# Optimization experiments

Measured on AMD Instinct MI355X. Metric: run time of the kernel, lower is better.

The kernel has to match this reference:

```python
import jax, jax.numpy as jnp
import numpy as np

N, E, G = 50000, 800000, 64
NODE_DIM, HID, HEADS, EDGE_DIM = 128, 256, 4, 2
LAYER_IN = [NODE_DIM, HID, HID]
LAYER_HEADS = [HEADS, HEADS, 1]
BN_EPS = 1e-5


def setup_inputs() -> dict:
    key = jax.random.key(0)
    ks = iter(jax.random.split(key, 80))
    def nrm(shape, s=0.05):
        return jax.random.normal(next(ks), shape, jnp.float32) * s
    inp = {}
    inp['x'] = jax.random.normal(next(ks), (N, NODE_DIM), jnp.float32)
    inp['edge_index'] = jax.random.randint(next(ks), (2, E), 0, N, jnp.int32)
    inp['edge_attr'] = jax.random.normal(next(ks), (E, EDGE_DIM), jnp.float32)
    inp['batch'] = jnp.sort(jax.random.randint(next(ks), (N,), 0, G, jnp.int32))
    for i in range(3):
        H = LAYER_HEADS[i]; C = HID // H
        inp[f'W{i}'] = nrm((LAYER_IN[i], H * C))
        inp[f'asrc{i}'] = nrm((H, C))
        inp[f'adst{i}'] = nrm((H, C))
        inp[f'We{i}'] = nrm((EDGE_DIM, H * C))
        inp[f'aedge{i}'] = nrm((H, C))
        inp[f'bconv{i}'] = jnp.zeros((HID,), jnp.float32)
        inp[f'bn{i}_g'] = jnp.ones((HID,), jnp.float32)
        inp[f'bn{i}_b'] = jnp.zeros((HID,), jnp.float32)
        inp[f'bn{i}_m'] = nrm((HID,), 0.01)
        inp[f'bn{i}_v'] = jnp.ones((HID,), jnp.float32)
    inp['Wskip'] = nrm((NODE_DIM, HID))
    inp['bskip'] = jnp.zeros((HID,), jnp.float32)
    inp['Wp1'] = nrm((2 * HID, HID))
    inp['bp1'] = jnp.zeros((HID,), jnp.float32)
    inp['Wp2'] = nrm((HID, 1))
    inp['bp2'] = jnp.zeros((1,), jnp.float32)
    return inp


def gat_conv(x, src, dst, ea, W, a_s, a_d, We, a_e, b, H, concat):
    n = x.shape[0]
    C = W.shape[1] // H
    h = (x @ W).reshape(n, H, C)                      # [N,H,C]
    # attention logits per edge (src/dst node terms + edge term)
    al = ((h * a_s).sum(-1)[src]
          + (h * a_d).sum(-1)[dst]
          + ((ea @ We).reshape(-1, H, C) * a_e).sum(-1))  # [Et,H]
    al = jax.nn.leaky_relu(al, 0.2)
    # segment softmax over destination nodes
    amax = jax.ops.segment_max(al, dst, num_segments=n)
    ex = jnp.exp(al - amax[dst])
    den = jax.ops.segment_sum(ex, dst, num_segments=n)
    alpha = ex / (den[dst] + 1e-16)
    out = jax.ops.segment_sum(h[src] * alpha[..., None], dst, num_segments=n)  # [N,H,C]
    out = out.reshape(n, H * C) if concat else out.mean(axis=1)
    return out + b


def _forward(x, edge_index, edge_attr, batch, layer_params, Wskip, bskip, Wp1, bp1, Wp2, bp2):
    n = x.shape[0]
    # add self-loops (PyG GATConv default), edge_attr filled with mean
    loop = jnp.arange(n, dtype=edge_index.dtype)
    src = jnp.concatenate([edge_index[0], loop])
    dst = jnp.concatenate([edge_index[1], loop])
    ea = jnp.concatenate([edge_attr, jnp.broadcast_to(edge_attr.mean(0), (n, edge_attr.shape[1]))], axis=0)
    identity = x
    for i, (W, a_s, a_d, We, a_e, b, g, be, rm, rv) in enumerate(layer_params):
        layer_identity = (identity @ Wskip + bskip) if i == 0 else identity
        concat = i < 2
        H = LAYER_HEADS[i]
        h = gat_conv(x, src, dst, ea, W, a_s, a_d, We, a_e, b, H, concat)
        h = (h - rm) * jax.lax.rsqrt(rv + BN_EPS) * g + be   # BatchNorm1d (eval)
        h = jax.nn.elu(h)
        x = h + layer_identity
        identity = x
    # global mean + max pool per graph
    counts = jnp.maximum(jax.ops.segment_sum(jnp.ones((n,), x.dtype), batch, num_segments=G), 1.0)
    mean_pool = jax.ops.segment_sum(x, batch, num_segments=G) / counts[:, None]
    max_pool = jax.ops.segment_max(x, batch, num_segments=G)
    emb = jnp.concatenate([mean_pool, max_pool], axis=1)      # [G, 2*HID]
    hmid = jax.nn.relu(emb @ Wp1 + bp1)
    return hmid @ Wp2 + bp2                                   # [G, 1]


def reference(x, edge_index, edge_attr, batch,
              W0, asrc0, adst0, We0, aedge0, bconv0, bn0_g, bn0_b, bn0_m, bn0_v,
              W1, asrc1, adst1, We1, aedge1, bconv1, bn1_g, bn1_b, bn1_m, bn1_v,
              W2, asrc2, adst2, We2, aedge2, bconv2, bn2_g, bn2_b, bn2_m, bn2_v,
              Wskip, bskip, Wp1, bp1, Wp2, bp2):
    layer_params = [
        (W0, asrc0, adst0, We0, aedge0, bconv0, bn0_g, bn0_b, bn0_m, bn0_v),
        (W1, asrc1, adst1, We1, aedge1, bconv1, bn1_g, bn1_b, bn1_m, bn1_v),
        (W2, asrc2, adst2, We2, aedge2, bconv2, bn2_g, bn2_b, bn2_m, bn2_v),
    ]
    return _forward(x, edge_index, edge_attr, batch, layer_params, Wskip, bskip, Wp1, bp1, Wp2, bp2)
```

## Files before the change

### kernel.cpp

```cpp
#include <hip/hip_runtime.h>
#include <cfloat>

#define Nn 50000
#define Ee 800000
#define Etot (Ee + Nn)
#define Gg 64
#define HIDc 256
#define BN_EPS 1e-5f

typedef unsigned int   uint32;
typedef unsigned short ushort16;
typedef short  bf16x8 __attribute__((ext_vector_type(8)));
typedef float  f32x4  __attribute__((ext_vector_type(4)));

__device__ inline ushort16 f2bf(float f) {
    uint32 u = __float_as_uint(f);
    u = (u + 0x7fffu + ((u >> 16) & 1u)) >> 16;
    return (ushort16)u;
}
__device__ inline uint32 pack2(float a, float b) {
    return (uint32)f2bf(a) | ((uint32)f2bf(b) << 16);
}
__device__ inline uint32 fenc(float f) {
    uint32 b = __float_as_uint(f);
    return (b & 0x80000000u) ? ~b : (b | 0x80000000u);
}
__device__ inline float fdec(uint32 u) {
    uint32 b = (u & 0x80000000u) ? (u & 0x7fffffffu) : ~u;
    return __uint_as_float(b);
}

__device__ inline long ws_index(int c, int k, int KB) {
    int cb = c >> 4, m = c & 15, kb = k >> 5, q = (k >> 3) & 3, e = k & 7;
    return (((long)(cb * KB + kb) * 64 + q * 16 + m) << 3) + e;
}

#define CVT4 (Nn * 128 / 4)
#define CVT_BLKS ((CVT4 + 255) / 256)
#define EBKS ((Etot + 255) / 256)
__global__ __launch_bounds__(256) void prep_kernel(
        const float* __restrict__ ea, float* __restrict__ ea_s,
        const float* __restrict__ We0, const float* __restrict__ ae0,
        const float* __restrict__ We1, const float* __restrict__ ae1,
        const float* __restrict__ We2, const float* __restrict__ ae2,
        float* __restrict__ M,
        const float* __restrict__ W0, const float* __restrict__ Wskip,
        const float* __restrict__ W1, const float* __restrict__ W2,
        ushort16* __restrict__ WtC, ushort16* __restrict__ Wt1,
        ushort16* __restrict__ Wt2,
        const float* __restrict__ x, ushort16* __restrict__ xbf,
        const int* __restrict__ ei, int* __restrict__ counts,
        const float* __restrict__ bc0, const float* __restrict__ g0,
        const float* __restrict__ b0, const float* __restrict__ m0,
        const float* __restrict__ v0,
        const float* __restrict__ bc1, const float* __restrict__ g1,
        const float* __restrict__ b1, const float* __restrict__ m1,
        const float* __restrict__ v1,
        const float* __restrict__ bc2, const float* __restrict__ g2,
        const float* __restrict__ b2, const float* __restrict__ m2,
        const float* __restrict__ v2,
        float* __restrict__ bnf) {
    int bid = blockIdx.x, t = threadIdx.x;
    if (bid < 256) {
        __shared__ float sh0[256], sh1[256];
        float s0 = 0.f, s1 = 0.f;
        for (int e = bid * 256 + t; e < Ee; e += 256 * 256) {
            s0 += ea[2 * e];
            s1 += ea[2 * e + 1];
        }
        sh0[t] = s0; sh1[t] = s1;
        __syncthreads();
        for (int off = 128; off > 0; off >>= 1) {
            if (t < off) { sh0[t] += sh0[t + off]; sh1[t] += sh1[t + off]; }
            __syncthreads();
        }
        if (t == 0) { atomicAdd(&ea_s[0], sh0[0]); atomicAdd(&ea_s[1], sh1[0]); }
    } else if (bid == 256) {
        if (t >= 18) return;
        int l = t < 8 ? 0 : (t < 16 ? 1 : 2);
        int r = t - l * 8;
        const float* We = (l == 0) ? We0 : (l == 1 ? We1 : We2);
        const float* ae = (l == 0) ? ae0 : (l == 1 ? ae1 : ae2);
        int Hl = (l < 2) ? 4 : 1;
        int Cl = 256 / Hl;
        int d = r / Hl, hh = r % Hl;
        float s = 0.f;
        for (int c = 0; c < Cl; ++c)
            s += We[d * 256 + hh * Cl + c] * ae[hh * Cl + c];
        M[l * 8 + r] = s;
    } else if (bid < 385) {
        int k = bid - 257;
        WtC[ws_index(t, k, 4)] = f2bf(W0[(long)k * 256 + t]);
    } else if (bid < 513) {
        int k = bid - 385;
        WtC[ws_index(256 + t, k, 4)] = f2bf(Wskip[(long)k * 256 + t]);
    } else if (bid < 769) {
        int k = bid - 513;
        Wt1[ws_index(t, k, 8)] = f2bf(W1[(long)k * 256 + t]);
    } else if (bid < 1025) {
        int k = bid - 769;
        Wt2[ws_index(t, k, 8)] = f2bf(W2[(long)k * 256 + t]);
    } else if (bid == 1025) {
        for (int ll = 0; ll < 3; ++ll) {
            const float* bc = ll == 0 ? bc0 : (ll == 1 ? bc1 : bc2);
            const float* gg = ll == 0 ? g0  : (ll == 1 ? g1  : g2);
            const float* bb = ll == 0 ? b0  : (ll == 1 ? b1  : b2);
            const float* mm = ll == 0 ? m0  : (ll == 1 ? m1  : m2);
            const float* vv = ll == 0 ? v0  : (ll == 1 ? v1  : v2);
            float s = gg[t] * rsqrtf(vv[t] + BN_EPS);
            bnf[ll * 512 + t]       = s;
            bnf[ll * 512 + 256 + t] = (bc[t] - mm[t]) * s + bb[t];
        }
    } else if (bid < 1026 + CVT_BLKS) {
        int i = (bid - 1026) * 256 + t;
        if (i < CVT4) {
            float4 v = *(const float4*)&x[i * 4];
            ushort4 o;
            o.x = f2bf(v.x); o.y = f2bf(v.y); o.z = f2bf(v.z); o.w = f2bf(v.w);
            *(ushort4*)&xbf[i * 4] = o;
        }
    } else {
        int e = (bid - 1026 - CVT_BLKS) * 256 + t;
        if (e < Etot) {
            int d = (e < Ee) ? ei[Ee + e] : (e - Ee);
            atomicAdd(&counts[d], 1);
        }
    }
}

__global__ void scan1_kernel(const int* __restrict__ in, int* __restrict__ inc,
                             int* __restrict__ bsums) {
    __shared__ int sh[256];
    int i = blockIdx.x * 256 + threadIdx.x;
    int v = (i < Nn) ? in[i] : 0;
    sh[threadIdx.x] = v;
    __syncthreads();
    for (int off = 1; off < 256; off <<= 1) {
        int t = ((int)threadIdx.x >= off) ? sh[threadIdx.x - off] : 0;
        __syncthreads();
        sh[threadIdx.x] += t;
        __syncthreads();
    }
    if (i < Nn) inc[i] = sh[threadIdx.x];
    if (threadIdx.x == 255) bsums[blockIdx.x] = sh[255];
}

__global__ void scan23_kernel(const int* __restrict__ inc, const int* __restrict__ bsums,
                              int* __restrict__ row_start, int* __restrict__ cursor, int nb) {
    __shared__ int sh[256];
    int b = blockIdx.x, t = threadIdx.x;
    sh[t] = (t < b && t < nb) ? bsums[t] : 0;
    __syncthreads();
    for (int off = 128; off > 0; off >>= 1) {
        if (t < off) sh[t] += sh[t + off];
        __syncthreads();
    }
    int base = sh[0];
    int i = b * 256 + t;
    if (i < Nn) {
        int v = inc[i] + base;
        row_start[i + 1] = v;
        cursor[i + 1] = v;
    }
    if (i == 0) { row_start[0] = 0; cursor[0] = 0; }
}

__global__ void scatter_kernel(const int* __restrict__ ei, const float* __restrict__ ea,
                               const float* __restrict__ ea_sum, int* __restrict__ cursor,
                               int* __restrict__ src_sorted, float* __restrict__ ea_sorted) {
    int e = blockIdx.x * blockDim.x + threadIdx.x;
    if (e >= Etot) return;
    int s, d; float e0, e1;
    if (e < Ee) {
        s = ei[e]; d = ei[Ee + e];
        e0 = ea[2 * e]; e1 = ea[2 * e + 1];
    } else {
        s = d = e - Ee;
        const float invE = 1.f / (float)Ee;
        e0 = ea_sum[0] * invE; e1 = ea_sum[1] * invE;
    }
    int pos = atomicAdd(&cursor[d], 1);
    src_sorted[pos] = s;
    ea_sorted[2 * pos]     = e0;
    ea_sorted[2 * pos + 1] = e1;
}

#define LDK0 136
__global__ __launch_bounds__(512) void mfma_gemm0_kernel(
        const ushort16* __restrict__ A,
        const ushort16* __restrict__ WS,
        uint32* __restrict__ outF, uint32* __restrict__ outS,
        const float* __restrict__ bskip,
        const float* __restrict__ a_s, const float* __restrict__ a_d,
        float* __restrict__ ssrc, float* __restrict__ sdst, int n) {
    __shared__ ushort16 As[128 * LDK0];
    const int t = threadIdx.x;
    const int row0 = blockIdx.x * 128;
    const int wave = t >> 6, lane = t & 63;
    const int wr = wave >> 2, wc = wave & 3;
    const int l15 = lane & 15, quad = lane >> 4;

    {
        int sm = t & 127, q4 = t >> 7;
        int grow = row0 + sm;
#pragma unroll
        for (int h = 0; h < 4; ++h) {
            int oct = q4 * 4 + h;
            uint4 va = make_uint4(0, 0, 0, 0);
            if (grow < n) va = *(const uint4*)&A[(long)grow * 128 + 8 * oct];
            *(uint4*)&As[sm * LDK0 + 8 * oct] = va;
        }
    }
    __syncthreads();

    for (int cc = 0; cc < 2; ++cc) {
        const int c0 = cc * 256;
        const bool isSkip = (cc == 1);
        f32x4 acc[4][4];
#pragma unroll
        for (int j = 0; j < 4; ++j)
#pragma unroll
            for (int i = 0; i < 4; ++i) {
                acc[j][i][0] = 0.f; acc[j][i][1] = 0.f;
                acc[j][i][2] = 0.f; acc[j][i][3] = 0.f;
            }
#pragma unroll
        for (int kb = 0; kb < 4; ++kb) {
            bf16x8 bfv[4];
#pragma unroll
            for (int j = 0; j < 4; ++j) {
                int cb = ((c0 + wc * 64) >> 4) + j;
                bfv[j] = *(const bf16x8*)&WS[(((long)cb * 4 + kb) * 64 + lane) << 3];
            }
            bf16x8 af[4];
#pragma unroll
            for (int i = 0; i < 4; ++i)
                af[i] = *(const bf16x8*)&As[(wr * 64 + i * 16 + l15) * LDK0
                                            + kb * 32 + quad * 8];
#pragma unroll
            for (int j = 0; j < 4; ++j)
#pragma unroll
                for (int i = 0; i < 4; ++i)
                    acc[j][i] = __builtin_amdgcn_mfma_f32_16x16x32_bf16(
                        bfv[j], af[i], acc[j][i], 0, 0, 0);
        }

        float4 bb[4];
#pragma unroll
        for (int j = 0; j < 4; ++j) {
            if (isSkip) bb[j] = *(const float4*)&bskip[wc * 64 + j * 16 + quad * 4];
            else        bb[j] = make_float4(0.f, 0.f, 0.f, 0.f);
        }
        uint32* tgt = isSkip ? outS : outF;
#pragma unroll
        for (int i = 0; i < 4; ++i) {
            int row = row0 + wr * 64 + i * 16 + l15;
            if (row >= n) continue;
#pragma unroll
            for (int j = 0; j < 4; ++j) {
                int col = wc * 64 + j * 16 + quad * 4;
                uint2 pk;
                pk.x = pack2(acc[j][i][0] + bb[j].x, acc[j][i][1] + bb[j].y);
                pk.y = pack2(acc[j][i][2] + bb[j].z, acc[j][i][3] + bb[j].w);
                *(uint2*)&tgt[(long)row * 128 + (col >> 1)] = pk;
            }
        }

        if (!isSkip) {
            float4 asv[4], adv[4];
#pragma unroll
            for (int j = 0; j < 4; ++j) {
                int col = wc * 64 + j * 16 + quad * 4;
                asv[j] = *(const float4*)&a_s[col];
                adv[j] = *(const float4*)&a_d[col];
            }
#pragma unroll
            for (int i = 0; i < 4; ++i) {
                float ps = 0.f, pd = 0.f;
#pragma unroll
                for (int j = 0; j < 4; ++j) {
                    ps += acc[j][i][0] * asv[j].x + acc[j][i][1] * asv[j].y
                        + acc[j][i][2] * asv[j].z + acc[j][i][3] * asv[j].w;
                    pd += acc[j][i][0] * adv[j].x + acc[j][i][1] * adv[j].y
                        + acc[j][i][2] * adv[j].z + acc[j][i][3] * adv[j].w;
                }
                ps += __shfl_xor(ps, 16); ps += __shfl_xor(ps, 32);
                pd += __shfl_xor(pd, 16); pd += __shfl_xor(pd, 32);
                if (quad == 0) {
                    int row = row0 + wr * 64 + i * 16 + l15;
                    if (row < n) {
                        ssrc[row * 4 + wc] = ps;
                        sdst[row * 4 + wc] = pd;
                    }
                }
            }
        }
    }
}

#define LDK 40
__global__ __launch_bounds__(512) void mfma_gemm12_kernel(
        const ushort16* __restrict__ A,
        const ushort16* __restrict__ WS,
        uint32* __restrict__ outF,
        const float* __restrict__ a_s, const float* __restrict__ a_d,
        float* __restrict__ ssrc, float* __restrict__ sdst, int n) {
    __shared__ ushort16 As[128 * LDK];
    const int t = threadIdx.x;
    const int row0 = blockIdx.x * 128;
    const int wave = t >> 6, lane = t & 63;
    const int wr = wave >> 2, wc = wave & 3;
    const int l15 = lane & 15, quad = lane >> 4;
    const int sm = t & 127, so = t >> 7;

    f32x4 acc[4][4];
#pragma unroll
    for (int j = 0; j < 4; ++j)
#pragma unroll
        for (int i = 0; i < 4; ++i) {
            acc[j][i][0] = 0.f; acc[j][i][1] = 0.f;
            acc[j][i][2] = 0.f; acc[j][i][3] = 0.f;
        }

    for (int kb = 0; kb < 8; ++kb) {
        {
            int grow = row0 + sm;
            uint4 va = make_uint4(0, 0, 0, 0);
            if (grow < n) va = *(const uint4*)&A[(long)grow * 256 + kb * 32 + 8 * so];
            *(uint4*)&As[sm * LDK + 8 * so] = va;
        }
        bf16x8 bfv[4];
#pragma unroll
        for (int j = 0; j < 4; ++j) {
            int cb = wc * 4 + j;
            bfv[j] = *(const bf16x8*)&WS[(((long)cb * 8 + kb) * 64 + lane) << 3];
        }
        __syncthreads();
        bf16x8 af[4];
#pragma unroll
        for (int i = 0; i < 4; ++i)
            af[i] = *(const bf16x8*)&As[(wr * 64 + i * 16 + l15) * LDK + quad * 8];
#pragma unroll
        for (int j = 0; j < 4; ++j)
#pragma unroll
            for (int i = 0; i < 4; ++i)
                acc[j][i] = __builtin_amdgcn_mfma_f32_16x16x32_bf16(
                    bfv[j], af[i], acc[j][i], 0, 0, 0);
        __syncthreads();
    }

#pragma unroll
    for (int i = 0; i < 4; ++i) {
        int row = row0 + wr * 64 + i * 16 + l15;
        if (row >= n) continue;
#pragma unroll
        for (int j = 0; j < 4; ++j) {
            int col = wc * 64 + j * 16 + quad * 4;
            uint2 pk;
            pk.x = pack2(acc[j][i][0], acc[j][i][1]);
            pk.y = pack2(acc[j][i][2], acc[j][i][3]);
            *(uint2*)&outF[(long)row * 128 + (col >> 1)] = pk;
        }
    }

    {
        float4 asv[4], adv[4];
#pragma unroll
        for (int j = 0; j < 4; ++j) {
            int col = wc * 64 + j * 16 + quad * 4;
            asv[j] = *(const float4*)&a_s[col];
            adv[j] = *(const float4*)&a_d[col];
        }
#pragma unroll
        for (int i = 0; i < 4; ++i) {
            float ps = 0.f, pd = 0.f;
#pragma unroll
            for (int j = 0; j < 4; ++j) {
                ps += acc[j][i][0] * asv[j].x + acc[j][i][1] * asv[j].y
                    + acc[j][i][2] * asv[j].z + acc[j][i][3] * asv[j].w;
                pd += acc[j][i][0] * adv[j].x + acc[j][i][1] * adv[j].y
                    + acc[j][i][2] * adv[j].z + acc[j][i][3] * adv[j].w;
            }
            ps += __shfl_xor(ps, 16); ps += __shfl_xor(ps, 32);
            pd += __shfl_xor(pd, 16); pd += __shfl_xor(pd, 32);
            if (quad == 0) {
                int row = row0 + wr * 64 + i * 16 + l15;
                if (row < n) {
                    ssrc[row * 4 + wc] = ps;
                    sdst[row * 4 + wc] = pd;
                }
            }
        }
    }
}

template <int H>
__global__ __launch_bounds__(256) void agg_fused_kernel(
        const int* __restrict__ src_sorted, const int* __restrict__ row_start,
        const float* __restrict__ ea_sorted, const float* __restrict__ ssrc,
        const float* __restrict__ sdst, const float* __restrict__ M,
        const uint32* __restrict__ hbuf2,
        const float* __restrict__ bnS, const float* __restrict__ bnB,
        const uint32* __restrict__ identity2, uint32* __restrict__ out2) {
    __shared__ int   s_sh[4][64];
    __shared__ float w_sh[4][64 * H];
    const int wv = threadIdx.x >> 6;
    const int l  = threadIdx.x & 63;
    const int node = blockIdx.x * 4 + wv;
    if (node >= Nn) return;
    const int hh = (H == 4) ? (l >> 4) : 0;
    const int beg = row_start[node], end = row_start[node + 1];

    const int c = 4 * l;
    const float4 scv = *(const float4*)&bnS[c];
    const float4 sbv = *(const float4*)&bnB[c];
    const uint2  idu = *(const uint2*)&identity2[(long)node * 128 + 2 * l];

    float M0[H], M1[H], sd[H];
    {
        float4 sdv = *(const float4*)&sdst[node * 4];
        if (H == 4) { sd[0] = sdv.x; sd[1] = sdv.y; sd[2] = sdv.z; sd[3] = sdv.w; }
        else         sd[0] = sdv.x + sdv.y + sdv.z + sdv.w;
#pragma unroll
        for (int h = 0; h < H; ++h) { M0[h] = M[h]; M1[h] = M[H + h]; }
    }

    float a0 = 0.f, a1 = 0.f, a2 = 0.f, a3 = 0.f, dnl = 0.f;
    const uint32 loff = (uint32)l << 3;

    for (int cb = beg; cb < end; cb += 64) {
        const int  el  = cb + l;
        const bool act = el < end;
        const int  elc = min(el, end - 1);
        const int  s   = src_sorted[elc];
        const float2 ev = *(const float2*)&ea_sorted[2 * elc];
        const float4 sv = *(const float4*)&ssrc[s * 4];
        if (cb != beg)
            asm volatile("s_waitcnt lgkmcnt(0)" ::: "memory");
        s_sh[wv][l] = s;
        if (H == 4) {
            float4 w4;
#pragma unroll
            for (int h = 0; h < 4; ++h) {
                float lg = ((const float*)&sv)[h] + sd[h]
                         + ev.x * M0[h] + ev.y * M1[h];
                lg = (lg > 0.f) ? lg : 0.2f * lg;
                ((float*)&w4)[h] = act ? __expf(lg) : 0.f;
            }
            *(float4*)&w_sh[wv][l * 4] = w4;
        } else {
            float lg = (sv.x + sv.y + sv.z + sv.w) + sd[0]
                     + ev.x * M0[0] + ev.y * M1[0];
            lg = (lg > 0.f) ? lg : 0.2f * lg;
            w_sh[wv][l] = act ? __expf(lg) : 0.f;
        }
        asm volatile("s_waitcnt lgkmcnt(0)" ::: "memory");

        const int cnt = min(64, end - cb);
        for (int base = 0; base < cnt; base += 16) {
            int sk[16]; float wk[16]; uint2 f[16];
#pragma unroll
            for (int k = 0; k < 16; ++k) {
                sk[k] = s_sh[wv][base + k];
                wk[k] = w_sh[wv][(base + k) * H + hh];
            }
#pragma unroll
            for (int k = 0; k < 16; ++k)
                f[k] = *(const uint2*)((const char*)hbuf2 +
                                       (((uint32)sk[k] << 9) + loff));
#pragma unroll
            for (int k = 0; k < 16; ++k) {
                float ww = wk[k];
                dnl += ww;
                a0 += ww * __uint_as_float(f[k].x << 16);
                a1 += ww * __uint_as_float(f[k].x & 0xffff0000u);
                a2 += ww * __uint_as_float(f[k].y << 16);
                a3 += ww * __uint_as_float(f[k].y & 0xffff0000u);
            }
        }
    }

    const float inv = 1.f / (dnl + 1e-16f);
    float v0 = a0 * (scv.x * inv) + sbv.x;
    float v1 = a1 * (scv.y * inv) + sbv.y;
    float v2 = a2 * (scv.z * inv) + sbv.z;
    float v3 = a3 * (scv.w * inv) + sbv.w;
    v0 = (v0 > 0.f) ? v0 : (expf(v0) - 1.f);
    v1 = (v1 > 0.f) ? v1 : (expf(v1) - 1.f);
    v2 = (v2 > 0.f) ? v2 : (expf(v2) - 1.f);
    v3 = (v3 > 0.f) ? v3 : (expf(v3) - 1.f);
    v0 += __uint_as_float(idu.x << 16);
    v1 += __uint_as_float(idu.x & 0xffff0000u);
    v2 += __uint_as_float(idu.y << 16);
    v3 += __uint_as_float(idu.y & 0xffff0000u);
    uint2 o;
    o.x = pack2(v0, v1);
    o.y = pack2(v2, v3);
    *(uint2*)&out2[(long)node * 128 + 2 * l] = o;
}

#define POOL_ROWS 32
__global__ __launch_bounds__(128) void pool_kernel(
        const uint32* __restrict__ x2, const int* __restrict__ batch,
        float* __restrict__ psum, uint32* __restrict__ pmax, float* __restrict__ pcnt) {
    int c2 = threadIdx.x;
    int n0 = blockIdx.x * POOL_ROWS;
    if (n0 >= Nn) return;
    int n1 = min(n0 + POOL_ROWS, Nn);
    int cur = batch[n0];
    float s0 = 0.f, s1 = 0.f, m0 = -FLT_MAX, m1 = -FLT_MAX;
    int cnt = 0;
    int c = 2 * c2;
    for (int i = n0; i < n1; ++i) {
        int g = batch[i];
        if (g != cur) {
            atomicAdd(&psum[cur * 256 + c], s0);
            atomicAdd(&psum[cur * 256 + c + 1], s1);
            atomicMax(&pmax[cur * 256 + c], fenc(m0));
            atomicMax(&pmax[cur * 256 + c + 1], fenc(m1));
            if (c2 == 0) atomicAdd(&pcnt[cur], (float)cnt);
            cur = g; s0 = s1 = 0.f; m0 = m1 = -FLT_MAX; cnt = 0;
        }
        uint32 u = x2[(long)i * 128 + c2];
        float lo = __uint_as_float(u << 16);
        float hi = __uint_as_float(u & 0xffff0000u);
        s0 += lo; s1 += hi;
        m0 = fmaxf(m0, lo); m1 = fmaxf(m1, hi);
        ++cnt;
    }
    atomicAdd(&psum[cur * 256 + c], s0);
    atomicAdd(&psum[cur * 256 + c + 1], s1);
    atomicMax(&pmax[cur * 256 + c], fenc(m0));
    atomicMax(&pmax[cur * 256 + c + 1], fenc(m1));
    if (c2 == 0) atomicAdd(&pcnt[cur], (float)cnt);
}

__global__ __launch_bounds__(256) void mlp_kernel(
        const float* __restrict__ psum, const uint32* __restrict__ pmax,
        const float* __restrict__ pcnt, const float* __restrict__ Wp1,
        const float* __restrict__ bp1, const float* __restrict__ Wp2,
        const float* __restrict__ bp2, float* __restrict__ out) {
    int g = blockIdx.x;
    int j = threadIdx.x;
    float inv = 1.f / fmaxf(pcnt[g], 1.f);
    float acc = bp1[j];
    for (int k = 0; k < 256; ++k)
        acc += (psum[g * 256 + k] * inv) * Wp1[k * 256 + j];
    for (int k = 0; k < 256; ++k)
        acc += fdec(pmax[g * 256 + k]) * Wp1[(256 + k) * 256 + j];
    float v = fmaxf(acc, 0.f) * Wp2[j];
    __shared__ float red[256];
    red[j] = v;
    __syncthreads();
    for (int off = 128; off > 0; off >>= 1) {
        if (j < off) red[j] += red[j + off];
        __syncthreads();
    }
    if (j == 0) out[g] = red[0] + bp2[0];
}

extern "C" void kernel_launch(void* const* d_in, const int* in_sizes, int n_in,
                              void* d_out, int out_size, void* d_ws, size_t ws_size,
                              hipStream_t stream) {
    const float* x   = (const float*)d_in[0];
    const int*   ei  = (const int*)d_in[1];
    const float* ea  = (const float*)d_in[2];
    const int*   bat = (const int*)d_in[3];
    auto LP = [&](int l, int j) { return (const float*)d_in[4 + l * 10 + j]; };
    const float* Wskip = (const float*)d_in[34];
    const float* bskip = (const float*)d_in[35];
    const float* Wp1   = (const float*)d_in[36];
    const float* bp1   = (const float*)d_in[37];
    const float* Wp2   = (const float*)d_in[38];
    const float* bp2   = (const float*)d_in[39];
    float* out = (float*)d_out;

    char* p = (char*)d_ws;
    auto alloc = [&](size_t bytes) { void* r = (void*)p; p += (bytes + 255) & ~(size_t)255; return r; };
    uint32*   hbuf2  = (uint32*)alloc((size_t)Nn * 256 * 2);
    uint32*   skipbf = (uint32*)alloc((size_t)Nn * 128 * 4);
    uint32*   resA   = (uint32*)alloc((size_t)Nn * 128 * 4);
    uint32*   resB   = (uint32*)alloc((size_t)Nn * 128 * 4);
    ushort16* xbf    = (ushort16*)alloc((size_t)Nn * 128 * 2);
    float*    ea_sorted = (float*)alloc((size_t)Etot * 2 * 4);
    float*    ssrc   = (float*)alloc((size_t)Nn * 4 * 4);
    float*    sdst   = (float*)alloc((size_t)Nn * 4 * 4);
    int*      counts = (int*)alloc((size_t)Nn * 4);
    int*      incb   = (int*)alloc((size_t)Nn * 4);
    int*      row_start = (int*)alloc((size_t)(Nn + 1) * 4);
    int*      cursor    = (int*)alloc((size_t)(Nn + 1) * 4);
    int*      src_sorted = (int*)alloc((size_t)Etot * 4);
    int*      bsums  = (int*)alloc(256 * 4);
    float*    ea_s   = (float*)alloc(2 * 4);
    float*    Mbuf   = (float*)alloc(32 * 4);
    float*    bnf    = (float*)alloc((size_t)3 * 512 * 4);
    ushort16* WtC    = (ushort16*)alloc((size_t)512 * 128 * 2);
    ushort16* Wt1    = (ushort16*)alloc((size_t)256 * 256 * 2);
    ushort16* Wt2    = (ushort16*)alloc((size_t)256 * 256 * 2);
    float*    psum   = (float*)alloc((size_t)Gg * 256 * 4);
    uint32*   pmax   = (uint32*)alloc((size_t)Gg * 256 * 4);
    float*    pcnt   = (float*)alloc((size_t)Gg * 4);

    const int nb = (Nn + 255) / 256;

    hipMemsetAsync(counts, 0, (size_t)Nn * 4, stream);
    hipMemsetAsync(ea_s, 0, 8, stream);
    hipMemsetAsync(psum, 0, (size_t)Gg * 256 * 4 * 2 + (size_t)Gg * 4, stream);

    prep_kernel<<<1026 + CVT_BLKS + EBKS, 256, 0, stream>>>(
        ea, ea_s, LP(0,3), LP(0,4), LP(1,3), LP(1,4), LP(2,3), LP(2,4), Mbuf,
        LP(0,0), Wskip, LP(1,0), LP(2,0), WtC, Wt1, Wt2, x, xbf, ei, counts,
        LP(0,5), LP(0,6), LP(0,7), LP(0,8), LP(0,9),
        LP(1,5), LP(1,6), LP(1,7), LP(1,8), LP(1,9),
        LP(2,5), LP(2,6), LP(2,7), LP(2,8), LP(2,9),
        bnf);

    scan1_kernel<<<nb, 256, 0, stream>>>(counts, incb, bsums);
    scan23_kernel<<<nb, 256, 0, stream>>>(incb, bsums, row_start, cursor, nb);
    scatter_kernel<<<EBKS, 256, 0, stream>>>(ei, ea, ea_s, cursor, src_sorted, ea_sorted);

    mfma_gemm0_kernel<<<(Nn + 127) / 128, 512, 0, stream>>>(
        xbf, WtC, hbuf2, skipbf, bskip,
        LP(0,1), LP(0,2), ssrc, sdst, Nn);

    const uint32* lid[3] = { skipbf, resA, resB };
    uint32*       lou[3] = { resA, resB, resA };
    const ushort16* lain[3] = { nullptr, (ushort16*)resA, (ushort16*)resB };
    const ushort16* lwt[3]  = { nullptr, Wt1, Wt2 };
    for (int l = 0; l < 3; ++l) {
        if (l > 0) {
            mfma_gemm12_kernel<<<(Nn + 127) / 128, 512, 0, stream>>>(
                lain[l], lwt[l], hbuf2,
                LP(l,1), LP(l,2), ssrc, sdst, Nn);
        }
        if (l < 2)
            agg_fused_kernel<4><<<(Nn + 3) / 4, 256, 0, stream>>>(
                src_sorted, row_start, ea_sorted, ssrc, sdst, Mbuf + l * 8,
                hbuf2, bnf + l * 512, bnf + l * 512 + 256,
                lid[l], lou[l]);
        else
            agg_fused_kernel<1><<<(Nn + 3) / 4, 256, 0, stream>>>(
                src_sorted, row_start, ea_sorted, ssrc, sdst, Mbuf + l * 8,
                hbuf2, bnf + l * 512, bnf + l * 512 + 256,
                lid[l], lou[l]);
    }

    pool_kernel<<<(Nn + POOL_ROWS - 1) / POOL_ROWS, 128, 0, stream>>>(resA, bat, psum, pmax, pcnt);
    mlp_kernel<<<Gg, 256, 0, stream>>>(psum, pmax, pcnt, Wp1, bp1, Wp2, bp2, out);
}
```

Measured before the change: 603.9 us.

## Split aggregation across 8 feature slices per node and pack edge records

The GAT aggregation kernel now launches 8 blocks per node group. Each wave covers one 32-channel slice, handles 4 edges in parallel across lane groups, and combines the partial sums with shuffles. Source index and edge attributes are packed into one 8-byte record per edge, storing the two edge features as bf16, which replaces separate src and ea arrays. This is meant to raise parallelism and cut per-edge metadata traffic. In exchange, metadata reads and logit computation are repeated for every slice. Packing the source index into 16 bits is unsafe for N=50000 only if it exceeds 65535, which it does not, but the edge attributes lose precision.

Measured after the change: 844.4 us. +39.8%, slower.

```diff
diff --git a/kernel.cpp b/kernel.cpp
--- a/kernel.cpp
+++ b/kernel.cpp
@@ -167,7 +167,7 @@
 
 __global__ void scatter_kernel(const int* __restrict__ ei, const float* __restrict__ ea,
                                const float* __restrict__ ea_sum, int* __restrict__ cursor,
-                               int* __restrict__ src_sorted, float* __restrict__ ea_sorted) {
+                               uint2* __restrict__ epk) {
     int e = blockIdx.x * blockDim.x + threadIdx.x;
     if (e >= Etot) return;
     int s, d; float e0, e1;
@@ -180,9 +180,10 @@
         e0 = ea_sum[0] * invE; e1 = ea_sum[1] * invE;
     }
     int pos = atomicAdd(&cursor[d], 1);
-    src_sorted[pos] = s;
-    ea_sorted[2 * pos]     = e0;
-    ea_sorted[2 * pos + 1] = e1;
+    uint2 r;
+    r.x = (uint32)s | ((uint32)f2bf(e0) << 16);
+    r.y = (uint32)f2bf(e1);
+    epk[pos] = r;
 }
 
 #define LDK0 136
@@ -396,107 +397,98 @@
 
 template <int H>
 __global__ __launch_bounds__(256) void agg_fused_kernel(
-        const int* __restrict__ src_sorted, const int* __restrict__ row_start,
-        const float* __restrict__ ea_sorted, const float* __restrict__ ssrc,
+        const uint2* __restrict__ epk, const int* __restrict__ row_start,
+        const float* __restrict__ ssrc,
         const float* __restrict__ sdst, const float* __restrict__ M,
         const uint32* __restrict__ hbuf2,
         const float* __restrict__ bnS, const float* __restrict__ bnB,
         const uint32* __restrict__ identity2, uint32* __restrict__ out2) {
     __shared__ int   s_sh[4][64];
-    __shared__ float w_sh[4][64 * H];
+    __shared__ float w_sh[4][64];
     const int wv = threadIdx.x >> 6;
     const int l  = threadIdx.x & 63;
-    const int node = blockIdx.x * 4 + wv;
+    const int slice = blockIdx.x & 7;
+    const int node = (blockIdx.x >> 3) * 4 + wv;
     if (node >= Nn) return;
-    const int hh = (H == 4) ? (l >> 4) : 0;
+    const int hh = (H == 4) ? (slice >> 1) : 0;
+    const int e4 = l >> 4, ch = l & 15;
     const int beg = row_start[node], end = row_start[node + 1];
 
-    const int c = 4 * l;
-    const float4 scv = *(const float4*)&bnS[c];
-    const float4 sbv = *(const float4*)&bnB[c];
-    const uint2  idu = *(const uint2*)&identity2[(long)node * 128 + 2 * l];
-
-    float M0[H], M1[H], sd[H];
-    {
+    const int c = slice * 32 + 2 * ch;
+    const float2 scv = *(const float2*)&bnS[c];
+    const float2 sbv = *(const float2*)&bnB[c];
+    const uint32 idu = identity2[(long)node * 128 + slice * 16 + ch];
+
+    const float M0 = M[hh], M1 = M[H + hh];
+    float sd;
+    if (H == 4) sd = sdst[node * 4 + hh];
+    else {
         float4 sdv = *(const float4*)&sdst[node * 4];
-        if (H == 4) { sd[0] = sdv.x; sd[1] = sdv.y; sd[2] = sdv.z; sd[3] = sdv.w; }
-        else         sd[0] = sdv.x + sdv.y + sdv.z + sdv.w;
-#pragma unroll
-        for (int h = 0; h < H; ++h) { M0[h] = M[h]; M1[h] = M[H + h]; }
-    }
-
-    float a0 = 0.f, a1 = 0.f, a2 = 0.f, a3 = 0.f, dnl = 0.f;
-    const uint32 loff = (uint32)l << 3;
+        sd = sdv.x + sdv.y + sdv.z + sdv.w;
+    }
+
+    float a0 = 0.f, a1 = 0.f, dnl = 0.f;
+    const uint32 loff = (uint32)(slice * 64 + ch * 4);
 
     for (int cb = beg; cb < end; cb += 64) {
         const int  el  = cb + l;
         const bool act = el < end;
         const int  elc = min(el, end - 1);
-        const int  s   = src_sorted[elc];
-        const float2 ev = *(const float2*)&ea_sorted[2 * elc];
-        const float4 sv = *(const float4*)&ssrc[s * 4];
+        const uint2 ep = epk[elc];
+        const int   s  = (int)(ep.x & 0xffffu);
+        const float e0 = __uint_as_float(ep.x & 0xffff0000u);
+        const float e1 = __uint_as_float(ep.y << 16);
+        float ss;
+        if (H == 4) ss = ssrc[s * 4 + hh];
+        else {
+            float4 sv = *(const float4*)&ssrc[s * 4];
+            ss = sv.x + sv.y + sv.z + sv.w;
+        }
         if (cb != beg)
             asm volatile("s_waitcnt lgkmcnt(0)" ::: "memory");
+        float lg = ss + sd + e0 * M0 + e1 * M1;
+        lg = (lg > 0.f) ? lg : 0.2f * lg;
         s_sh[wv][l] = s;
-        if (H == 4) {
-            float4 w4;
-#pragma unroll
-            for (int h = 0; h < 4; ++h) {
-                float lg = ((const float*)&sv)[h] + sd[h]
-                         + ev.x * M0[h] + ev.y * M1[h];
-                lg = (lg > 0.f) ? lg : 0.2f * lg;
-                ((float*)&w4)[h] = act ? __expf(lg) : 0.f;
-            }
-            *(float4*)&w_sh[wv][l * 4] = w4;
-        } else {
-            float lg = (sv.x + sv.y + sv.z + sv.w) + sd[0]
-                     + ev.x * M0[0] + ev.y * M1[0];
-            lg = (lg > 0.f) ? lg : 0.2f * lg;
-            w_sh[wv][l] = act ? __expf(lg) : 0.f;
-        }
+        w_sh[wv][l] = act ? __expf(lg) : 0.f;
         asm volatile("s_waitcnt lgkmcnt(0)" ::: "memory");
 
         const int cnt = min(64, end - cb);
         for (int base = 0; base < cnt; base += 16) {
-            int sk[16]; float wk[16]; uint2 f[16];
-#pragma unroll
-            for (int k = 0; k < 16; ++k) {
-                sk[k] = s_sh[wv][base + k];
-                wk[k] = w_sh[wv][(base + k) * H + hh];
-            }
-#pragma unroll
-            for (int k = 0; k < 16; ++k)
-                f[k] = *(const uint2*)((const char*)hbuf2 +
-                                       (((uint32)sk[k] << 9) + loff));
-#pragma unroll
-            for (int k = 0; k < 16; ++k) {
+            int sk[4]; float wk[4]; uint32 f[4];
+#pragma unroll
+            for (int k = 0; k < 4; ++k) {
+                int idx = base + k * 4 + e4;
+                sk[k] = s_sh[wv][idx];
+                wk[k] = w_sh[wv][idx];
+            }
+#pragma unroll
+            for (int k = 0; k < 4; ++k)
+                f[k] = *(const uint32*)((const char*)hbuf2 +
+                                        (((uint32)sk[k] << 9) + loff));
+#pragma unroll
+            for (int k = 0; k < 4; ++k) {
                 float ww = wk[k];
                 dnl += ww;
-                a0 += ww * __uint_as_float(f[k].x << 16);
-                a1 += ww * __uint_as_float(f[k].x & 0xffff0000u);
-                a2 += ww * __uint_as_float(f[k].y << 16);
-                a3 += ww * __uint_as_float(f[k].y & 0xffff0000u);
-            }
-        }
-    }
-
-    const float inv = 1.f / (dnl + 1e-16f);
-    float v0 = a0 * (scv.x * inv) + sbv.x;
-    float v1 = a1 * (scv.y * inv) + sbv.y;
-    float v2 = a2 * (scv.z * inv) + sbv.z;
-    float v3 = a3 * (scv.w * inv) + sbv.w;
-    v0 = (v0 > 0.f) ? v0 : (expf(v0) - 1.f);
-    v1 = (v1 > 0.f) ? v1 : (expf(v1) - 1.f);
-    v2 = (v2 > 0.f) ? v2 : (expf(v2) - 1.f);
-    v3 = (v3 > 0.f) ? v3 : (expf(v3) - 1.f);
-    v0 += __uint_as_float(idu.x << 16);
-    v1 += __uint_as_float(idu.x & 0xffff0000u);
-    v2 += __uint_as_float(idu.y << 16);
-    v3 += __uint_as_float(idu.y & 0xffff0000u);
-    uint2 o;
-    o.x = pack2(v0, v1);
-    o.y = pack2(v2, v3);
-    *(uint2*)&out2[(long)node * 128 + 2 * l] = o;
+                a0 += ww * __uint_as_float(f[k] << 16);
+                a1 += ww * __uint_as_float(f[k] & 0xffff0000u);
+            }
+        }
+    }
+
+    a0 += __shfl_xor(a0, 16); a0 += __shfl_xor(a0, 32);
+    a1 += __shfl_xor(a1, 16); a1 += __shfl_xor(a1, 32);
+    dnl += __shfl_xor(dnl, 16); dnl += __shfl_xor(dnl, 32);
+
+    if (e4 == 0) {
+        const float inv = 1.f / (dnl + 1e-16f);
+        float v0 = a0 * (scv.x * inv) + sbv.x;
+        float v1 = a1 * (scv.y * inv) + sbv.y;
+        v0 = (v0 > 0.f) ? v0 : (expf(v0) - 1.f);
+        v1 = (v1 > 0.f) ? v1 : (expf(v1) - 1.f);
+        v0 += __uint_as_float(idu << 16);
+        v1 += __uint_as_float(idu & 0xffff0000u);
+        out2[(long)node * 128 + slice * 16 + ch] = pack2(v0, v1);
+    }
 }
 
 #define POOL_ROWS 32
@@ -582,14 +574,13 @@
     uint32*   resA   = (uint32*)alloc((size_t)Nn * 128 * 4);
     uint32*   resB   = (uint32*)alloc((size_t)Nn * 128 * 4);
     ushort16* xbf    = (ushort16*)alloc((size_t)Nn * 128 * 2);
-    float*    ea_sorted = (float*)alloc((size_t)Etot * 2 * 4);
+    uint2*    epk    = (uint2*)alloc((size_t)Etot * 8);
     float*    ssrc   = (float*)alloc((size_t)Nn * 4 * 4);
     float*    sdst   = (float*)alloc((size_t)Nn * 4 * 4);
     int*      counts = (int*)alloc((size_t)Nn * 4);
     int*      incb   = (int*)alloc((size_t)Nn * 4);
     int*      row_start = (int*)alloc((size_t)(Nn + 1) * 4);
     int*      cursor    = (int*)alloc((size_t)(Nn + 1) * 4);
-    int*      src_sorted = (int*)alloc((size_t)Etot * 4);
     int*      bsums  = (int*)alloc(256 * 4);
     float*    ea_s   = (float*)alloc(2 * 4);
     float*    Mbuf   = (float*)alloc(32 * 4);
@@ -617,12 +608,13 @@
 
     scan1_kernel<<<nb, 256, 0, stream>>>(counts, incb, bsums);
     scan23_kernel<<<nb, 256, 0, stream>>>(incb, bsums, row_start, cursor, nb);
-    scatter_kernel<<<EBKS, 256, 0, stream>>>(ei, ea, ea_s, cursor, src_sorted, ea_sorted);
+    scatter_kernel<<<EBKS, 256, 0, stream>>>(ei, ea, ea_s, cursor, epk);
 
     mfma_gemm0_kernel<<<(Nn + 127) / 128, 512, 0, stream>>>(
         xbf, WtC, hbuf2, skipbf, bskip,
         LP(0,1), LP(0,2), ssrc, sdst, Nn);
 
+    const int agrid = ((Nn + 3) / 4) * 8;
     const uint32* lid[3] = { skipbf, resA, resB };
     uint32*       lou[3] = { resA, resB, resA };
     const ushort16* lain[3] = { nullptr, (ushort16*)resA, (ushort16*)resB };
@@ -634,13 +626,13 @@
                 LP(l,1), LP(l,2), ssrc, sdst, Nn);
         }
         if (l < 2)
-            agg_fused_kernel<4><<<(Nn + 3) / 4, 256, 0, stream>>>(
-                src_sorted, row_start, ea_sorted, ssrc, sdst, Mbuf + l * 8,
+            agg_fused_kernel<4><<<agrid, 256, 0, stream>>>(
+                epk, row_start, ssrc, sdst, Mbuf + l * 8,
                 hbuf2, bnf + l * 512, bnf + l * 512 + 256,
                 lid[l], lou[l]);
         else
-            agg_fused_kernel<1><<<(Nn + 3) / 4, 256, 0, stream>>>(
-                src_sorted, row_start, ea_sorted, ssrc, sdst, Mbuf + l * 8,
+            agg_fused_kernel<1><<<agrid, 256, 0, stream>>>(
+                epk, row_start, ssrc, sdst, Mbuf + l * 8,
                 hbuf2, bnf + l * 512, bnf + l * 512 + 256,
                 lid[l], lou[l]);
     }
```
